# Kernel tuning notes

Hardware: AMD Instinct MI355X
Metric: run time of the kernel (lower is better)

## Reference

```python
import jax, jax.numpy as jnp
import numpy as np

B, S, DIM = 2, 2048, 2048
NUM_HEADS, HEAD_DIM, KV_PER = 16, 128, 1
NUM_KV = NUM_HEADS * KV_PER  # = 16; code requires KV_PER == 1 for shape consistency
QKV_OUT = (NUM_HEADS + 2 * NUM_KV) * HEAD_DIM


def setup_inputs() -> dict:
    key = jax.random.key(0)
    k1, k2, k3 = jax.random.split(key, 3)
    x = jax.random.normal(k1, (B, S, DIM), dtype=jnp.float32)
    w_qkv = jax.random.normal(k2, (DIM, QKV_OUT), dtype=jnp.float32) * (DIM ** -0.5)
    w_out = jax.random.normal(k3, (NUM_HEADS * HEAD_DIM, DIM), dtype=jnp.float32) * ((NUM_HEADS * HEAD_DIM) ** -0.5)
    return {"x": x, "w_qkv": w_qkv, "w_out": w_out}


def reference(x, w_qkv, w_out):
    b, s, _ = x.shape
    # QKV projection, then split heads: [b, s, nq + 2*nkv, d]
    qkv = (x @ w_qkv).reshape(b, s, NUM_HEADS + 2 * NUM_KV, HEAD_DIM)
    q = qkv[:, :, :NUM_HEADS]                          # [b, s, nq, d]
    k = qkv[:, :, NUM_HEADS:NUM_HEADS + NUM_KV]        # [b, s, nkv, d]
    v = qkv[:, :, NUM_HEADS + NUM_KV:]                 # [b, s, nkv, d]
    # query -> [b, nkv, per, s, d] (per == KV_PER == 1)
    q = q.reshape(b, s, NUM_KV, KV_PER, HEAD_DIM).transpose(0, 2, 3, 1, 4)
    k = k.transpose(0, 2, 1, 3)                        # [b, nkv, s, d]
    v = v.transpose(0, 2, 1, 3)                        # [b, nkv, s, d]
    scale = 1.0 / (HEAD_DIM ** 0.5)
    # logits: [b, nkv, per, s_q, s_k]
    logits = jnp.einsum('bkpsd,bktd->bkpst', q, k) * scale
    attn = jax.nn.softmax(logits.astype(jnp.float32), axis=-1)
    # combined: [b, nkv, per, s, d] -> [b, s, nkv, per, d] -> [b, s, dim]
    combined = jnp.einsum('bkpst,bktd->bkpsd', attn, v.astype(jnp.float32)).astype(v.dtype)
    combined = combined.transpose(0, 3, 1, 2, 4).reshape(b, s, NUM_KV * KV_PER * HEAD_DIM)
    return combined @ w_out
```

## Files before the change

### kernel.cpp

```cpp
#include <hip/hip_runtime.h>
#include <cstdint>

typedef __bf16 bf16x8 __attribute__((ext_vector_type(8)));
typedef float f32x4 __attribute__((ext_vector_type(4)));
typedef unsigned short u16x8 __attribute__((ext_vector_type(8)));

#define NH 16
#define HD 128
#define SEQ 2048
#define DIM 2048
#define QKVO 6144

__device__ __forceinline__ unsigned short f32_bf16(float f) {
  uint32_t u = __builtin_bit_cast(uint32_t, f);
  u += 0x7fffu + ((u >> 16) & 1u);
  return (unsigned short)(u >> 16);
}

__device__ __forceinline__ void gl2lds16(const void* g, void* l) {
  __builtin_amdgcn_global_load_lds(
      (const __attribute__((address_space(1))) uint32_t*)g,
      (__attribute__((address_space(3))) uint32_t*)l,
      16, 0, 0);
}

__global__ __launch_bounds__(256) void cvt_f32_bf16(
    const float* __restrict__ in, unsigned short* __restrict__ out) {
  long i = ((long)blockIdx.x * 256 + threadIdx.x) * 8;
  f32x4 a = *(const f32x4*)(in + i);
  f32x4 b = *(const f32x4*)(in + i + 4);
  u16x8 r;
#pragma unroll
  for (int j = 0; j < 4; j++) { r[j] = f32_bf16(a[j]); r[4 + j] = f32_bf16(b[j]); }
  *(u16x8*)(out + i) = r;
}

__global__ __launch_bounds__(256) void transpose_f32_bf16(
    const float* __restrict__ in, unsigned short* __restrict__ out,
    int R, int C) {
  __shared__ unsigned short tile[64][65];
  const int t = threadIdx.x, tx = t & 63, ty = t >> 6;
  const long r0 = (long)blockIdx.y * 64, c0 = (long)blockIdx.x * 64;
  for (int i = 0; i < 16; i++) {
    int row = ty + i * 4;
    tile[row][tx] = f32_bf16(in[(r0 + row) * C + c0 + tx]);
  }
  __syncthreads();
  for (int i = 0; i < 16; i++) {
    int row = ty + i * 4;
    out[(c0 + row) * R + r0 + tx] = tile[tx][row];
  }
}

__global__ __launch_bounds__(256) void transpose_v(
    const unsigned short* __restrict__ qkv, unsigned short* __restrict__ vT) {
  __shared__ unsigned short tile[64][65];
  const int t = threadIdx.x, tx = t & 63, ty = t >> 6;
  const int bh = blockIdx.z, b = bh >> 4, h = bh & 15;
  const long t0 = (long)blockIdx.x * 64;
  const int d0 = blockIdx.y * 64;
  const unsigned short* src = qkv + (long)b * SEQ * QKVO + 2 * NH * HD + h * HD;
  for (int i = 0; i < 16; i++) {
    int row = ty + i * 4;
    tile[row][tx] = src[(t0 + row) * QKVO + d0 + tx];
  }
  __syncthreads();
  unsigned short* dst = vT + ((long)bh * HD + d0) * SEQ + t0;
  for (int i = 0; i < 16; i++) {
    int row = ty + i * 4;
    dst[(long)row * SEQ + tx] = tile[tx][row];
  }
}

template <typename OutT>
__global__ __launch_bounds__(256) void gemm_bt(
    const unsigned short* __restrict__ A, int lda,
    const unsigned short* __restrict__ BT, int ldb,
    OutT* __restrict__ C, int ldc, int K) {
  __shared__ __align__(16) unsigned short As[128 * 32];
  __shared__ __align__(16) unsigned short Bs[128 * 32];
  const int t = threadIdx.x;
  const int lane = t & 63, w = t >> 6;
  const int quad = lane >> 4, l16 = lane & 15;
  const int wm = (w & 1) * 64, wn = (w >> 1) * 64;
  const long m0 = (long)blockIdx.y * 128, n0 = (long)blockIdx.x * 128;

  f32x4 acc[4][4] = {};
  const int rowA = t >> 2, kslot = (t & 3) * 8;
  const unsigned short* Ag = A + (m0 + rowA) * (long)lda + kslot;
  const unsigned short* Bg = BT + (n0 + rowA) * (long)ldb + kslot;
  unsigned short* AsBase = &As[w * 512];
  unsigned short* BsBase = &Bs[w * 512];

  for (int k0 = 0; k0 < K; k0 += 32) {
    __syncthreads();
    gl2lds16(Ag + k0, AsBase);
    gl2lds16(Ag + 64 * (long)lda + k0, AsBase + 2048);
    gl2lds16(Bg + k0, BsBase);
    gl2lds16(Bg + 64 * (long)ldb + k0, BsBase + 2048);
    __syncthreads();

    bf16x8 af[4], bf[4];
#pragma unroll
    for (int mt = 0; mt < 4; mt++)
      af[mt] = *(const bf16x8*)&As[(wm + mt * 16 + l16) * 32 + quad * 8];
#pragma unroll
    for (int nt = 0; nt < 4; nt++)
      bf[nt] = *(const bf16x8*)&Bs[(wn + nt * 16 + l16) * 32 + quad * 8];
#pragma unroll
    for (int mt = 0; mt < 4; mt++)
#pragma unroll
      for (int nt = 0; nt < 4; nt++)
        acc[mt][nt] = __builtin_amdgcn_mfma_f32_16x16x32_bf16(
            af[mt], bf[nt], acc[mt][nt], 0, 0, 0);
  }

#pragma unroll
  for (int mt = 0; mt < 4; mt++) {
    long row = m0 + wm + mt * 16 + quad * 4;
#pragma unroll
    for (int r = 0; r < 4; r++) {
      OutT* crow = C + (row + r) * (long)ldc + n0 + wn + l16;
#pragma unroll
      for (int nt = 0; nt < 4; nt++) {
        float v = acc[mt][nt][r];
        if constexpr (sizeof(OutT) == 2) crow[nt * 16] = f32_bf16(v);
        else                             crow[nt * 16] = v;
      }
    }
  }
}

#define KSTR 136
#define VSTR 72
__global__ __launch_bounds__(256, 2) void attn_kernel(
    unsigned short* qkv, const unsigned short* __restrict__ vT) {
  __shared__ __align__(16) unsigned short Ks[64 * KSTR];
  __shared__ __align__(16) unsigned short Vs[128 * VSTR];
  __shared__ __align__(16) unsigned short Ps[4][32 * VSTR];

  const int t = threadIdx.x, lane = t & 63, w = t >> 6;
  const int quad = lane >> 4, l16 = lane & 15;
  const int q0 = blockIdx.x * 128, h = blockIdx.y, b = blockIdx.z;
  const long row0 = (long)b * SEQ;

  bf16x8 qf[2][4];
#pragma unroll
  for (int mt = 0; mt < 2; mt++) {
    const unsigned short* Qp =
        qkv + (row0 + q0 + w * 32 + mt * 16 + l16) * (long)QKVO + h * HD + quad * 8;
#pragma unroll
    for (int c = 0; c < 4; c++) qf[mt][c] = *(const bf16x8*)(Qp + c * 32);
  }

  float m_i[2][4], l_i[2][4];
  f32x4 o[2][8] = {};
#pragma unroll
  for (int mt = 0; mt < 2; mt++)
#pragma unroll
    for (int r = 0; r < 4; r++) { m_i[mt][r] = -1e30f; l_i[mt][r] = 0.f; }
  const float sm_scale = 0.08838834764831845f * 1.4426950408889634f;

  const unsigned short* Kg = qkv + row0 * QKVO + NH * HD + h * HD;
  const unsigned short* Vg = vT + ((long)(b * NH + h)) * HD * SEQ;

  bf16x8 kr[4], vr[4];
#pragma unroll
  for (int i = 0; i < 4; i++) {
    int s = i * 256 + t;
    kr[i] = *(const bf16x8*)(Kg + (long)(s >> 4) * QKVO + (s & 15) * 8);
  }
#pragma unroll
  for (int i = 0; i < 4; i++) {
    int s = i * 256 + t;
    vr[i] = *(const bf16x8*)(Vg + (long)(s >> 3) * SEQ + (s & 7) * 8);
  }

  for (int kc = 0; kc < SEQ; kc += 64) {
    __syncthreads();
#pragma unroll
    for (int i = 0; i < 4; i++) {
      int s = i * 256 + t;
      *(bf16x8*)&Ks[(s >> 4) * KSTR + (s & 15) * 8] = kr[i];
    }
#pragma unroll
    for (int i = 0; i < 4; i++) {
      int s = i * 256 + t;
      *(bf16x8*)&Vs[(s >> 3) * VSTR + (s & 7) * 8] = vr[i];
    }
    __syncthreads();

    if (kc + 64 < SEQ) {
#pragma unroll
      for (int i = 0; i < 4; i++) {
        int s = i * 256 + t;
        kr[i] = *(const bf16x8*)(Kg + (long)(kc + 64 + (s >> 4)) * QKVO + (s & 15) * 8);
      }
#pragma unroll
      for (int i = 0; i < 4; i++) {
        int s = i * 256 + t;
        vr[i] = *(const bf16x8*)(Vg + (long)(s >> 3) * SEQ + kc + 64 + (s & 7) * 8);
      }
    }

    f32x4 s4[2][4];
#pragma unroll
    for (int kt = 0; kt < 4; kt++) {
      f32x4 a0 = {}, a1 = {};
#pragma unroll
      for (int c = 0; c < 4; c++) {
        bf16x8 kf = *(const bf16x8*)&Ks[(kt * 16 + l16) * KSTR + c * 32 + quad * 8];
        a0 = __builtin_amdgcn_mfma_f32_16x16x32_bf16(qf[0][c], kf, a0, 0, 0, 0);
        a1 = __builtin_amdgcn_mfma_f32_16x16x32_bf16(qf[1][c], kf, a1, 0, 0, 0);
      }
      s4[0][kt] = a0; s4[1][kt] = a1;
    }

#pragma unroll
    for (int mt = 0; mt < 2; mt++)
#pragma unroll
      for (int r = 0; r < 4; r++) {
        float v0 = s4[mt][0][r] * sm_scale, v1 = s4[mt][1][r] * sm_scale;
        float v2 = s4[mt][2][r] * sm_scale, v3 = s4[mt][3][r] * sm_scale;
        float mx = fmaxf(fmaxf(v0, v1), fmaxf(v2, v3));
#pragma unroll
        for (int d = 1; d < 16; d <<= 1) mx = fmaxf(mx, __shfl_xor(mx, d, 64));
        float mn = fmaxf(m_i[mt][r], mx);
        float alpha = exp2f(m_i[mt][r] - mn);
        m_i[mt][r] = mn;
        float p0 = exp2f(v0 - mn), p1 = exp2f(v1 - mn);
        float p2 = exp2f(v2 - mn), p3 = exp2f(v3 - mn);
        s4[mt][0][r] = p0; s4[mt][1][r] = p1; s4[mt][2][r] = p2; s4[mt][3][r] = p3;
        float ls = (p0 + p1) + (p2 + p3);
#pragma unroll
        for (int d = 1; d < 16; d <<= 1) ls += __shfl_xor(ls, d, 64);
        l_i[mt][r] = l_i[mt][r] * alpha + ls;
#pragma unroll
        for (int dt = 0; dt < 8; dt++) o[mt][dt][r] *= alpha;
      }

#pragma unroll
    for (int mt = 0; mt < 2; mt++)
#pragma unroll
      for (int kt = 0; kt < 4; kt++)
#pragma unroll
        for (int r = 0; r < 4; r++)
          Ps[w][(mt * 16 + quad * 4 + r) * VSTR + kt * 16 + l16] = f32_bf16(s4[mt][kt][r]);
    asm volatile("s_waitcnt lgkmcnt(0)" ::: "memory");

#pragma unroll
    for (int cc = 0; cc < 2; cc++) {
      bf16x8 pf0 = *(const bf16x8*)&Ps[w][(l16) * VSTR + cc * 32 + quad * 8];
      bf16x8 pf1 = *(const bf16x8*)&Ps[w][(16 + l16) * VSTR + cc * 32 + quad * 8];
#pragma unroll
      for (int dt = 0; dt < 8; dt++) {
        bf16x8 vf = *(const bf16x8*)&Vs[(dt * 16 + l16) * VSTR + cc * 32 + quad * 8];
        o[0][dt] = __builtin_amdgcn_mfma_f32_16x16x32_bf16(pf0, vf, o[0][dt], 0, 0, 0);
        o[1][dt] = __builtin_amdgcn_mfma_f32_16x16x32_bf16(pf1, vf, o[1][dt], 0, 0, 0);
      }
    }
  }

#pragma unroll
  for (int mt = 0; mt < 2; mt++) {
    long orow = row0 + q0 + w * 32 + mt * 16 + quad * 4;
    unsigned short* Op = qkv + orow * (long)QKVO + h * HD + l16;
#pragma unroll
    for (int r = 0; r < 4; r++) {
      float inv = 1.f / l_i[mt][r];
#pragma unroll
      for (int dt = 0; dt < 8; dt++)
        Op[(long)r * QKVO + dt * 16] = f32_bf16(o[mt][dt][r] * inv);
    }
  }
}

extern "C" void kernel_launch(void* const* d_in, const int* in_sizes, int n_in,
                              void* d_out, int out_size, void* d_ws, size_t ws_size,
                              hipStream_t stream) {
  const float* x     = (const float*)d_in[0];
  const float* w_qkv = (const float*)d_in[1];
  const float* w_out = (const float*)d_in[2];
  float* out = (float*)d_out;

  char* ws = (char*)d_ws;
  unsigned short* qkv   = (unsigned short*)ws;
  unsigned short* xbf   = (unsigned short*)(ws + 50331648);
  unsigned short* wqkvT = (unsigned short*)(ws + 67108864);
  unsigned short* vTbuf = (unsigned short*)(ws + 67108864);
  unsigned short* woutT = (unsigned short*)(ws + 83886080);

  dim3 blk(256);
  cvt_f32_bf16<<<4096, blk, 0, stream>>>(x, xbf);
  transpose_f32_bf16<<<dim3(QKVO / 64, DIM / 64), blk, 0, stream>>>(w_qkv, wqkvT, DIM, QKVO);
  gemm_bt<unsigned short><<<dim3(QKVO / 128, 4096 / 128), blk, 0, stream>>>(
      xbf, DIM, wqkvT, DIM, qkv, QKVO, DIM);
  transpose_v<<<dim3(SEQ / 64, HD / 64, 2 * NH), blk, 0, stream>>>(qkv, vTbuf);
  transpose_f32_bf16<<<dim3(DIM / 64, DIM / 64), blk, 0, stream>>>(w_out, woutT, DIM, DIM);
  attn_kernel<<<dim3(SEQ / 128, NH, 2), blk, 0, stream>>>(qkv, vTbuf);
  gemm_bt<float><<<dim3(DIM / 128, 4096 / 128), blk, 0, stream>>>(
      qkv, QKVO, woutT, DIM, out, DIM, DIM);
}
```

Measured before the change: 493.4 us.

## Transpose QK^T MFMA, lazy softmax rescale, packed bf16 P stores

Swaps the MFMA operands so each lane holds one query row's scores across keys. This reduces the row max and row sum to two cross-quad shuffles instead of four butterfly steps per row. Online-softmax rescaling of O now runs only when some row's max grows beyond a threshold (the FA4-style lazy rescale), and the scale is folded into an fma before exp2. P is packed with v_cvt_pk_bf16_f32 and written to LDS as 8-byte stores, replacing per-element scalar stores. The risk is a wave-divergent branch and fp32 overflow headroom, bounded by the threshold of 2^8.

Measured after the change: 430.6 us. -12.7%, faster.

```diff
diff --git a/kernel.cpp b/kernel.cpp
--- a/kernel.cpp
+++ b/kernel.cpp
@@ -15,6 +15,12 @@
   uint32_t u = __builtin_bit_cast(uint32_t, f);
   u += 0x7fffu + ((u >> 16) & 1u);
   return (unsigned short)(u >> 16);
+}
+
+__device__ __forceinline__ uint32_t cvt_pk_bf16(float a, float b) {
+  uint32_t r;
+  asm("v_cvt_pk_bf16_f32 %0, %1, %2" : "=v"(r) : "v"(a), "v"(b));
+  return r;
 }
 
 __device__ __forceinline__ void gl2lds16(const void* g, void* l) {
@@ -153,13 +159,12 @@
     for (int c = 0; c < 4; c++) qf[mt][c] = *(const bf16x8*)(Qp + c * 32);
   }
 
-  float m_i[2][4], l_i[2][4];
+  float m_l[2], l_l[2];
   f32x4 o[2][8] = {};
-#pragma unroll
-  for (int mt = 0; mt < 2; mt++)
-#pragma unroll
-    for (int r = 0; r < 4; r++) { m_i[mt][r] = -1e30f; l_i[mt][r] = 0.f; }
-  const float sm_scale = 0.08838834764831845f * 1.4426950408889634f;
+  m_l[0] = m_l[1] = -1e30f;
+  l_l[0] = l_l[1] = 0.f;
+  const float c2 = 0.08838834764831845f * 1.4426950408889634f;
+  const float thr = 8.0f / c2;
 
   const unsigned short* Kg = qkv + row0 * QKVO + NH * HD + h * HD;
   const unsigned short* Vg = vT + ((long)(b * NH + h)) * HD * SEQ;
@@ -203,49 +208,70 @@
       }
     }
 
-    f32x4 s4[2][4];
+    f32x4 st[2][4];
 #pragma unroll
     for (int kt = 0; kt < 4; kt++) {
       f32x4 a0 = {}, a1 = {};
 #pragma unroll
       for (int c = 0; c < 4; c++) {
         bf16x8 kf = *(const bf16x8*)&Ks[(kt * 16 + l16) * KSTR + c * 32 + quad * 8];
-        a0 = __builtin_amdgcn_mfma_f32_16x16x32_bf16(qf[0][c], kf, a0, 0, 0, 0);
-        a1 = __builtin_amdgcn_mfma_f32_16x16x32_bf16(qf[1][c], kf, a1, 0, 0, 0);
-      }
-      s4[0][kt] = a0; s4[1][kt] = a1;
-    }
-
-#pragma unroll
-    for (int mt = 0; mt < 2; mt++)
-#pragma unroll
-      for (int r = 0; r < 4; r++) {
-        float v0 = s4[mt][0][r] * sm_scale, v1 = s4[mt][1][r] * sm_scale;
-        float v2 = s4[mt][2][r] * sm_scale, v3 = s4[mt][3][r] * sm_scale;
-        float mx = fmaxf(fmaxf(v0, v1), fmaxf(v2, v3));
-#pragma unroll
-        for (int d = 1; d < 16; d <<= 1) mx = fmaxf(mx, __shfl_xor(mx, d, 64));
-        float mn = fmaxf(m_i[mt][r], mx);
-        float alpha = exp2f(m_i[mt][r] - mn);
-        m_i[mt][r] = mn;
-        float p0 = exp2f(v0 - mn), p1 = exp2f(v1 - mn);
-        float p2 = exp2f(v2 - mn), p3 = exp2f(v3 - mn);
-        s4[mt][0][r] = p0; s4[mt][1][r] = p1; s4[mt][2][r] = p2; s4[mt][3][r] = p3;
-        float ls = (p0 + p1) + (p2 + p3);
-#pragma unroll
-        for (int d = 1; d < 16; d <<= 1) ls += __shfl_xor(ls, d, 64);
-        l_i[mt][r] = l_i[mt][r] * alpha + ls;
-#pragma unroll
-        for (int dt = 0; dt < 8; dt++) o[mt][dt][r] *= alpha;
-      }
-
-#pragma unroll
-    for (int mt = 0; mt < 2; mt++)
-#pragma unroll
-      for (int kt = 0; kt < 4; kt++)
-#pragma unroll
-        for (int r = 0; r < 4; r++)
-          Ps[w][(mt * 16 + quad * 4 + r) * VSTR + kt * 16 + l16] = f32_bf16(s4[mt][kt][r]);
+        a0 = __builtin_amdgcn_mfma_f32_16x16x32_bf16(kf, qf[0][c], a0, 0, 0, 0);
+        a1 = __builtin_amdgcn_mfma_f32_16x16x32_bf16(kf, qf[1][c], a1, 0, 0, 0);
+      }
+      st[0][kt] = a0; st[1][kt] = a1;
+    }
+
+#pragma unroll
+    for (int mt = 0; mt < 2; mt++) {
+      float mx0 = fmaxf(fmaxf(st[mt][0][0], st[mt][0][1]),
+                        fmaxf(st[mt][0][2], st[mt][0][3]));
+      float mx1 = fmaxf(fmaxf(st[mt][1][0], st[mt][1][1]),
+                        fmaxf(st[mt][1][2], st[mt][1][3]));
+      float mx2 = fmaxf(fmaxf(st[mt][2][0], st[mt][2][1]),
+                        fmaxf(st[mt][2][2], st[mt][2][3]));
+      float mx3 = fmaxf(fmaxf(st[mt][3][0], st[mt][3][1]),
+                        fmaxf(st[mt][3][2], st[mt][3][3]));
+      float mx = fmaxf(fmaxf(mx0, mx1), fmaxf(mx2, mx3));
+      mx = fmaxf(mx, __shfl_xor(mx, 16, 64));
+      mx = fmaxf(mx, __shfl_xor(mx, 32, 64));
+
+      if (__any(mx > m_l[mt] + thr)) {
+        float mn = fmaxf(m_l[mt], mx);
+        float alpha = exp2f(c2 * (m_l[mt] - mn));
+        m_l[mt] = mn;
+        l_l[mt] *= alpha;
+        float a_o[4];
+#pragma unroll
+        for (int r = 0; r < 4; r++) a_o[r] = __shfl(alpha, (quad << 2) | r, 16);
+#pragma unroll
+        for (int dt = 0; dt < 8; dt++)
+#pragma unroll
+          for (int r = 0; r < 4; r++) o[mt][dt][r] *= a_o[r];
+      }
+
+      float cm = c2 * m_l[mt];
+      float sum = 0.f;
+      uint32_t pk0[4], pk1[4];
+#pragma unroll
+      for (int kt = 0; kt < 4; kt++) {
+        float p0 = exp2f(fmaf(st[mt][kt][0], c2, -cm));
+        float p1 = exp2f(fmaf(st[mt][kt][1], c2, -cm));
+        float p2 = exp2f(fmaf(st[mt][kt][2], c2, -cm));
+        float p3 = exp2f(fmaf(st[mt][kt][3], c2, -cm));
+        sum += (p0 + p1) + (p2 + p3);
+        pk0[kt] = cvt_pk_bf16(p0, p1);
+        pk1[kt] = cvt_pk_bf16(p2, p3);
+      }
+      sum += __shfl_xor(sum, 16, 64);
+      sum += __shfl_xor(sum, 32, 64);
+      l_l[mt] += sum;
+
+#pragma unroll
+      for (int kt = 0; kt < 4; kt++) {
+        uint2 w2; w2.x = pk0[kt]; w2.y = pk1[kt];
+        *(uint2*)&Ps[w][(mt * 16 + l16) * VSTR + kt * 16 + quad * 4] = w2;
+      }
+    }
     asm volatile("s_waitcnt lgkmcnt(0)" ::: "memory");
 
 #pragma unroll
@@ -261,16 +287,22 @@
     }
   }
 
+  float inv_o[2][4];
+#pragma unroll
+  for (int mt = 0; mt < 2; mt++) {
+    float linv = 1.f / l_l[mt];
+#pragma unroll
+    for (int r = 0; r < 4; r++) inv_o[mt][r] = __shfl(linv, (quad << 2) | r, 16);
+  }
 #pragma unroll
   for (int mt = 0; mt < 2; mt++) {
     long orow = row0 + q0 + w * 32 + mt * 16 + quad * 4;
     unsigned short* Op = qkv + orow * (long)QKVO + h * HD + l16;
 #pragma unroll
     for (int r = 0; r < 4; r++) {
-      float inv = 1.f / l_i[mt][r];
 #pragma unroll
       for (int dt = 0; dt < 8; dt++)
-        Op[(long)r * QKVO + dt * 16] = f32_bf16(o[mt][dt][r] * inv);
+        Op[(long)r * QKVO + dt * 16] = f32_bf16(o[mt][dt][r] * inv_o[mt][r]);
     }
   }
 }
```
